# Kernel optimization log

Measured on AMD Instinct MI355X. Metric: run time of the kernel, lower is better.

Reference implementation:

```python
import jax, jax.numpy as jnp
import numpy as np

B, N, C, O, R = 8, 1024, 768, 768, 16  # batch, tokens, in_features, out_features, rank


def setup_inputs() -> dict:
    key = jax.random.key(0)
    k1, k2, k3, k4 = jax.random.split(key, 4)
    x = jax.random.normal(k1, (B, N, C), dtype=jnp.float32)
    coef = jax.random.normal(k2, (N, R), dtype=jnp.float32)
    # params: weight (out_features, in_features, rank), bias (out_features, rank)
    weight = 0.02 * jax.random.normal(k3, (O, C, R), dtype=jnp.float32)
    bias = 0.02 * jax.random.normal(k4, (O, R), dtype=jnp.float32)
    return {"x": x, "coef": coef, "weight": weight, "bias": bias}


def reference(x, coef, weight, bias):
    # Original math: per-token weight W_n[o,c] = sum_r coef[n,r] * weight[o,c,r]
    #                out[b,n,o] = sum_c x[b,n,c] * W_n[o,c] + sum_r coef[n,r]*bias[o,r]
    # Fused form: contract in_features first, rank last; avoids the (N,O,C) tensor.
    t = jnp.einsum('bnc,ocr->bnor', x, weight)   # (B,N,O,R)
    out = jnp.einsum('bnor,nr->bno', t, coef)    # (B,N,O)
    out = out + coef @ bias.T                    # (N,O) broadcast over batch
    return out
```

## Files before the change

### kernel.cpp

```cpp
#include <hip/hip_runtime.h>

#define BB 8
#define NN 1024
#define CC 768
#define OO 768
#define RR 16
#define MM (BB*NN)
#define KK (CC*RR)
#define BM 128
#define BO 128
#define BK 64
#define KTILES (KK/BK)

typedef __bf16 bf16x8 __attribute__((ext_vector_type(8)));
typedef float  f32x4  __attribute__((ext_vector_type(4)));

__device__ static __forceinline__ void gl_lds16(const void* g, void* l) {
    __builtin_amdgcn_global_load_lds(
        (const __attribute__((address_space(1))) void*)g,
        (__attribute__((address_space(3))) void*)l,
        16, 0, 0);
}

__global__ __launch_bounds__(256) void k_prep(const float* __restrict__ w,
                                              const float* __restrict__ coef,
                                              const float* __restrict__ bias,
                                              __bf16* __restrict__ wbf,
                                              float* __restrict__ bterm) {
    long id = blockIdx.x;
    if (id < 4608) {
        long u = (id * 256 + threadIdx.x) * 8;
        float4 a = *(const float4*)(w + u);
        float4 b = *(const float4*)(w + u + 4);
        bf16x8 v = {(__bf16)a.x, (__bf16)a.y, (__bf16)a.z, (__bf16)a.w,
                    (__bf16)b.x, (__bf16)b.y, (__bf16)b.z, (__bf16)b.w};
        *(bf16x8*)(wbf + u) = v;
    } else {
        int i = (int)(id - 4608) * 256 + threadIdx.x;
        int n = i / OO, o = i - n * OO;
        float s = 0.f;
#pragma unroll
        for (int r = 0; r < RR; ++r) s += coef[n * RR + r] * bias[o * RR + r];
        bterm[i] = s;
    }
}

__global__ __launch_bounds__(256, 2) void k_gemm(const float* __restrict__ x,
                                                 const float* __restrict__ coef,
                                                 const __bf16* __restrict__ wbf,
                                                 const float* __restrict__ bterm,
                                                 float* __restrict__ out) {
    __shared__ __bf16 lA[BM * BK];
    __shared__ __bf16 lB[BO * BK];

    const int tid = threadIdx.x;

    int id    = blockIdx.x;
    int xcd   = id & 7;
    int slot  = id >> 3;
    int otile = slot >> 3;
    int mtile = xcd * 8 + (slot & 7);
    const int m0 = mtile * BM, o0 = otile * BO;

    const int am     = tid & 127;
    const int ahalf  = tid >> 7;
    const int m_glob = m0 + am;
    const int n_idx  = m_glob & (NN - 1);
    const float* xrow = x + (long)m_glob * CC;

    float cf[16];
#pragma unroll
    for (int r = 0; r < 16; r += 4) {
        float4 t4 = *(const float4*)(coef + n_idx * RR + r);
        cf[r] = t4.x; cf[r + 1] = t4.y; cf[r + 2] = t4.z; cf[r + 3] = t4.w;
    }

    const int lane = tid & 63, wave = tid >> 6;
    const int wm = (wave & 1) * 64, wo = (wave >> 1) * 64;
    const int lrow = lane & 15, quad = lane >> 4;

    f32x4 acc[4][4] = {};

    float2 x2 = *(const float2*)(xrow + 2 * ahalf);

#pragma unroll 1
    for (int kt = 0; kt < KTILES; ++kt) {
#pragma unroll
        for (int s = 0; s < 4; ++s) {
            int u = s * 256 + tid;
            int row = u >> 3, cl = u & 7;
            int g = cl ^ (row & 7);
            const __bf16* gp = wbf + (long)(o0 + row) * KK + kt * BK + g * 8;
            gl_lds16(gp, ((char*)lB) + u * 16);
        }
        float2 x2n = x2;
        if (kt + 1 < KTILES) x2n = *(const float2*)(xrow + (kt + 1) * 4 + 2 * ahalf);
#pragma unroll
        for (int ci = 0; ci < 2; ++ci) {
            float xv = (ci == 0) ? x2.x : x2.y;
            int c_local = 2 * ahalf + ci;
#pragma unroll
            for (int rh = 0; rh < 2; ++rh) {
                bf16x8 v;
#pragma unroll
                for (int j = 0; j < 8; ++j) v[j] = (__bf16)(xv * cf[rh * 8 + j]);
                int kb  = c_local * 2 + rh;
                int kbs = kb ^ (am & 7);
                *(bf16x8*)(&lA[am * BK + kbs * 8]) = v;
            }
        }
        x2 = x2n;
        __syncthreads();

#pragma unroll
        for (int ks = 0; ks < 2; ++ks) {
            bf16x8 af[4], bfr[4];
            int kb = ks * 4 + quad;
#pragma unroll
            for (int im = 0; im < 4; ++im) {
                int row = wm + im * 16 + lrow;
                af[im] = *(const bf16x8*)(&lA[row * BK + (kb ^ (row & 7)) * 8]);
            }
#pragma unroll
            for (int io = 0; io < 4; ++io) {
                int row = wo + io * 16 + lrow;
                bfr[io] = *(const bf16x8*)(&lB[row * BK + (kb ^ (row & 7)) * 8]);
            }
#pragma unroll
            for (int im = 0; im < 4; ++im)
#pragma unroll
                for (int io = 0; io < 4; ++io)
                    acc[im][io] = __builtin_amdgcn_mfma_f32_16x16x32_bf16(
                        af[im], bfr[io], acc[im][io], 0, 0, 0);
        }
        __syncthreads();
    }

    const int nbase = m0 & (NN - 1);
#pragma unroll
    for (int im = 0; im < 4; ++im) {
#pragma unroll
        for (int io = 0; io < 4; ++io) {
            int o = o0 + wo + io * 16 + lrow;
#pragma unroll
            for (int r = 0; r < 4; ++r) {
                int moff = wm + im * 16 + quad * 4 + r;
                long m = m0 + moff;
                out[m * OO + o] = acc[im][io][r] + bterm[(nbase + moff) * OO + o];
            }
        }
    }
}

__global__ void k_naive(const float* __restrict__ x, const float* __restrict__ coef,
                        const float* __restrict__ w, const float* __restrict__ bias,
                        float* __restrict__ out) {
    long i = (long)blockIdx.x * 256 + threadIdx.x;
    if (i >= (long)MM * OO) return;
    int o = (int)(i % OO);
    long m = i / OO;
    int n = (int)(m & (NN - 1));
    float cf[16];
#pragma unroll
    for (int r = 0; r < 16; ++r) cf[r] = coef[n * RR + r];
    const float* xr = x + m * CC;
    const float* wr = w + (long)o * CC * RR;
    float s = 0.f;
    for (int c = 0; c < CC; ++c) {
        float t = 0.f;
#pragma unroll
        for (int r = 0; r < 16; ++r) t += cf[r] * wr[c * RR + r];
        s += xr[c] * t;
    }
    float bs = 0.f;
#pragma unroll
    for (int r = 0; r < 16; ++r) bs += cf[r] * bias[o * RR + r];
    out[i] = s + bs;
}

extern "C" void kernel_launch(void* const* d_in, const int* in_sizes, int n_in,
                              void* d_out, int out_size, void* d_ws, size_t ws_size,
                              hipStream_t stream) {
    const float* x    = (const float*)d_in[0];
    const float* coef = (const float*)d_in[1];
    const float* w    = (const float*)d_in[2];
    const float* bias = (const float*)d_in[3];
    float* out = (float*)d_out;

    const size_t wbf_bytes = (size_t)OO * KK * sizeof(__bf16);
    const size_t bt_bytes  = (size_t)NN * OO * sizeof(float);

    if (ws_size >= wbf_bytes + bt_bytes) {
        __bf16* wbf  = (__bf16*)d_ws;
        float*  btrm = (float*)((char*)d_ws + wbf_bytes);
        k_prep<<<7680, 256, 0, stream>>>(w, coef, bias, wbf, btrm);
        k_gemm<<<384, 256, 0, stream>>>(x, coef, wbf, btrm, out);
    } else {
        k_naive<<<(int)(((long)MM * OO + 255) / 256), 256, 0, stream>>>(x, coef, w, bias, out);
    }
}
```

Measured before the change: 284.1 us.

## Double-buffer LDS tiles, halve M tile, and remap blocks for a single wave

Moves the GEMM to double-buffered LDS. The weight tile and the x·coef A tile for step k+1 are staged while MFMAs run on step k, so only one barrier is needed per iteration. The M tile shrinks from 128 to 64, which doubles the grid to 768 blocks and raises the launch-bounds occupancy hint to 3 blocks per CU. This targets the tail imbalance of 384 blocks across the CUs. Blocks are remapped with an XCD-aware swizzle. The trade-off is that each block now does half the work per weight tile, so weight traffic through L2 doubles and the MFMA-to-load ratio drops.

```diff
diff --git a/kernel.cpp b/kernel.cpp
--- a/kernel.cpp
+++ b/kernel.cpp
@@ -7,10 +7,13 @@
 #define RR 16
 #define MM (BB*NN)
 #define KK (CC*RR)
-#define BM 128
+#define BM 64
 #define BO 128
 #define BK 64
 #define KTILES (KK/BK)
+#define MTILES (MM/BM)
+#define OTILES (OO/BO)
+#define NBLK (MTILES*OTILES)
 
 typedef __bf16 bf16x8 __attribute__((ext_vector_type(8)));
 typedef float  f32x4  __attribute__((ext_vector_type(4)));
@@ -45,25 +48,24 @@
     }
 }
 
-__global__ __launch_bounds__(256, 2) void k_gemm(const float* __restrict__ x,
+__global__ __launch_bounds__(256, 3) void k_gemm(const float* __restrict__ x,
                                                  const float* __restrict__ coef,
                                                  const __bf16* __restrict__ wbf,
                                                  const float* __restrict__ bterm,
                                                  float* __restrict__ out) {
-    __shared__ __bf16 lA[BM * BK];
-    __shared__ __bf16 lB[BO * BK];
+    __shared__ __bf16 lA[2][BM * BK];
+    __shared__ __bf16 lB[2][BO * BK];
 
     const int tid = threadIdx.x;
 
-    int id    = blockIdx.x;
-    int xcd   = id & 7;
-    int slot  = id >> 3;
-    int otile = slot >> 3;
-    int mtile = xcd * 8 + (slot & 7);
+    int bid  = blockIdx.x;
+    int swz  = (bid & 7) * (NBLK / 8) + (bid >> 3);
+    int otile = swz >> 7;
+    int mtile = swz & 127;
     const int m0 = mtile * BM, o0 = otile * BO;
 
-    const int am     = tid & 127;
-    const int ahalf  = tid >> 7;
+    const int am = tid & 63;
+    const int ac = tid >> 6;
     const int m_glob = m0 + am;
     const int n_idx  = m_glob & (NN - 1);
     const float* xrow = x + (long)m_glob * CC;
@@ -76,58 +78,64 @@
     }
 
     const int lane = tid & 63, wave = tid >> 6;
-    const int wm = (wave & 1) * 64, wo = (wave >> 1) * 64;
+    const int wr = wave & 1, wc = wave >> 1;
     const int lrow = lane & 15, quad = lane >> 4;
 
-    f32x4 acc[4][4] = {};
-
-    float2 x2 = *(const float2*)(xrow + 2 * ahalf);
-
-#pragma unroll 1
-    for (int kt = 0; kt < KTILES; ++kt) {
+    f32x4 acc[2][4] = {};
+
+    auto STAGE = [&](int b, int kt) {
 #pragma unroll
         for (int s = 0; s < 4; ++s) {
             int u = s * 256 + tid;
             int row = u >> 3, cl = u & 7;
             int g = cl ^ (row & 7);
             const __bf16* gp = wbf + (long)(o0 + row) * KK + kt * BK + g * 8;
-            gl_lds16(gp, ((char*)lB) + u * 16);
-        }
-        float2 x2n = x2;
-        if (kt + 1 < KTILES) x2n = *(const float2*)(xrow + (kt + 1) * 4 + 2 * ahalf);
-#pragma unroll
-        for (int ci = 0; ci < 2; ++ci) {
-            float xv = (ci == 0) ? x2.x : x2.y;
-            int c_local = 2 * ahalf + ci;
-#pragma unroll
-            for (int rh = 0; rh < 2; ++rh) {
-                bf16x8 v;
-#pragma unroll
-                for (int j = 0; j < 8; ++j) v[j] = (__bf16)(xv * cf[rh * 8 + j]);
-                int kb  = c_local * 2 + rh;
-                int kbs = kb ^ (am & 7);
-                *(bf16x8*)(&lA[am * BK + kbs * 8]) = v;
+            gl_lds16(gp, ((char*)lB[b]) + u * 16);
+        }
+    };
+    auto BUILD = [&](int b, float xv) {
+#pragma unroll
+        for (int rh = 0; rh < 2; ++rh) {
+            bf16x8 v;
+#pragma unroll
+            for (int j = 0; j < 8; ++j) v[j] = (__bf16)(xv * cf[rh * 8 + j]);
+            int kb  = ac * 2 + rh;
+            int kbs = kb ^ (am & 7);
+            *(bf16x8*)(&lA[b][am * BK + kbs * 8]) = v;
+        }
+    };
+
+    float xv = xrow[ac];
+    STAGE(0, 0);
+    float xn = xrow[4 + ac];
+    BUILD(0, xv);
+    __syncthreads();
+
+#pragma unroll 2
+    for (int kt = 0; kt < KTILES; ++kt) {
+        const int cur = kt & 1;
+        if (kt + 1 < KTILES) {
+            STAGE(cur ^ 1, kt + 1);
+            BUILD(cur ^ 1, xn);
+            int nc = (kt + 2 < KTILES) ? (kt + 2) : (KTILES - 1);
+            xn = xrow[nc * 4 + ac];
+        }
+#pragma unroll
+        for (int ks = 0; ks < 2; ++ks) {
+            bf16x8 af[2], bfr[4];
+            int kb = ks * 4 + quad;
+#pragma unroll
+            for (int im = 0; im < 2; ++im) {
+                int row = wr * 32 + im * 16 + lrow;
+                af[im] = *(const bf16x8*)(&lA[cur][row * BK + (kb ^ (row & 7)) * 8]);
             }
-        }
-        x2 = x2n;
-        __syncthreads();
-
-#pragma unroll
-        for (int ks = 0; ks < 2; ++ks) {
-            bf16x8 af[4], bfr[4];
-            int kb = ks * 4 + quad;
-#pragma unroll
-            for (int im = 0; im < 4; ++im) {
-                int row = wm + im * 16 + lrow;
-                af[im] = *(const bf16x8*)(&lA[row * BK + (kb ^ (row & 7)) * 8]);
+#pragma unroll
+            for (int io = 0; io < 4; ++io) {
+                int row = wc * 64 + io * 16 + lrow;
+                bfr[io] = *(const bf16x8*)(&lB[cur][row * BK + (kb ^ (row & 7)) * 8]);
             }
 #pragma unroll
-            for (int io = 0; io < 4; ++io) {
-                int row = wo + io * 16 + lrow;
-                bfr[io] = *(const bf16x8*)(&lB[row * BK + (kb ^ (row & 7)) * 8]);
-            }
-#pragma unroll
-            for (int im = 0; im < 4; ++im)
+            for (int im = 0; im < 2; ++im)
 #pragma unroll
                 for (int io = 0; io < 4; ++io)
                     acc[im][io] = __builtin_amdgcn_mfma_f32_16x16x32_bf16(
@@ -138,13 +146,13 @@
 
     const int nbase = m0 & (NN - 1);
 #pragma unroll
-    for (int im = 0; im < 4; ++im) {
+    for (int im = 0; im < 2; ++im) {
 #pragma unroll
         for (int io = 0; io < 4; ++io) {
-            int o = o0 + wo + io * 16 + lrow;
+            int o = o0 + wc * 64 + io * 16 + lrow;
 #pragma unroll
             for (int r = 0; r < 4; ++r) {
-                int moff = wm + im * 16 + quad * 4 + r;
+                int moff = wr * 32 + im * 16 + quad * 4 + r;
                 long m = m0 + moff;
                 out[m * OO + o] = acc[im][io][r] + bterm[(nbase + moff) * OO + o];
             }
@@ -194,7 +202,7 @@
         __bf16* wbf  = (__bf16*)d_ws;
         float*  btrm = (float*)((char*)d_ws + wbf_bytes);
         k_prep<<<7680, 256, 0, stream>>>(w, coef, bias, wbf, btrm);
-        k_gemm<<<384, 256, 0, stream>>>(x, coef, wbf, btrm, out);
+        k_gemm<<<NBLK, 256, 0, stream>>>(x, coef, wbf, btrm, out);
     } else {
         k_naive<<<(int)(((long)MM * OO + 255) / 256), 256, 0, stream>>>(x, coef, w, bias, out);
     }
```

New measurement: 296.9 us. 4.5% more time.
